# Kernel optimization log

Hardware: AMD Instinct MI355X
Metric: run time of the kernel (lower is better)

Reference implementation:

```python
import jax, jax.numpy as jnp
import numpy as np

D_MODEL = 1024
NHEAD = 16
HEAD_DIM = D_MODEL // NHEAD  # 64
THETA = 10000.0


def apply_rope(t):
    # t: [B, H, S, D]. Interleaved-pair RoPE (lucidrains rotary-embedding-torch
    # rotate_queries_or_keys), positions = arange(S), theta = 10000.
    B, H, S, D = t.shape
    inv_freq = 1.0 / (THETA ** (jnp.arange(0, D, 2, dtype=jnp.float32) / D))  # [D/2]
    ang = jnp.arange(S, dtype=jnp.float32)[:, None] * inv_freq               # [S, D/2]
    cos = jnp.cos(ang).astype(t.dtype)
    sin = jnp.sin(ang).astype(t.dtype)
    tp = t.reshape(B, H, S, D // 2, 2)
    x1, x2 = tp[..., 0], tp[..., 1]
    rot = jnp.stack([x1 * cos - x2 * sin, x1 * sin + x2 * cos], axis=-1)
    return rot.reshape(B, H, S, D)


def setup_inputs() -> dict:
    key = jax.random.key(0)
    k0, k1, k2, k3, k4 = jax.random.split(key, 5)
    B, Sx, Sc = 2, 2048, 2048
    sc = 0.02  # weight init scale
    return {
        "x": jax.random.normal(k0, (B, Sx, D_MODEL), jnp.float32),
        "context": jax.random.normal(k1, (B, Sc, D_MODEL), jnp.float32),
        "Wq": jax.random.normal(k2, (D_MODEL, D_MODEL), jnp.float32) * sc,
        "Wv": jax.random.normal(k3, (D_MODEL, D_MODEL), jnp.float32) * sc,
        "Wo": jax.random.normal(k4, (D_MODEL, D_MODEL), jnp.float32) * sc,
        "bo": jnp.zeros((D_MODEL,), jnp.float32),
        "x_pos": jnp.arange(B * Sx, dtype=jnp.int64).reshape(B, Sx) % Sx,
        "context_pos": jnp.arange(B * Sc, dtype=jnp.int64).reshape(B, Sc) % Sc,
    }


def reference(x, context, Wq, Wv, Wo, bo, x_pos, context_pos):
    # x_pos/context_pos are unused when both streams use the internal
    # RotaryEmbedding (is_imu1=is_imu2=True), matching the original forward.
    B, Sx, _ = x.shape
    Sc = context.shape[1]
    q = (x @ Wq.T).reshape(B, Sx, NHEAD, HEAD_DIM).transpose(0, 2, 1, 3)
    # NOTE: original code uses projq (not projk) for keys — replicated here.
    k = (context @ Wq.T).reshape(B, Sc, NHEAD, HEAD_DIM).transpose(0, 2, 1, 3)
    v = (context @ Wv.T).reshape(B, Sc, NHEAD, HEAD_DIM).transpose(0, 2, 1, 3)
    q = apply_rope(q)
    k = apply_rope(k)
    scale = 1.0 / jnp.sqrt(jnp.asarray(HEAD_DIM, q.dtype))
    attn = jax.nn.softmax(jnp.einsum("bhqd,bhkd->bhqk", q, k) * scale, axis=-1)
    out = jnp.einsum("bhqk,bhkd->bhqd", attn, v)            # [B,H,Sx,hd]
    out = out.transpose(0, 2, 1, 3).reshape(B, Sx, D_MODEL)  # [B,Sx,d_model]
    return out @ Wo.T + bo
```

## Files before the change

### kernel.cpp

```cpp
#include <hip/hip_runtime.h>
#include <cmath>


typedef __bf16 bf16x8 __attribute__((ext_vector_type(8)));
typedef __bf16 bf16x4 __attribute__((ext_vector_type(4)));
typedef float f32x4 __attribute__((ext_vector_type(4)));

#define MFMA(A, B, C) __builtin_amdgcn_mfma_f32_16x16x32_bf16(A, B, C, 0, 0, 0)
#define GLL16(g, l)                                                        \
  __builtin_amdgcn_global_load_lds(                                        \
      (const __attribute__((address_space(1))) unsigned int*)(g),          \
      (__attribute__((address_space(3))) unsigned int*)(l), 16, 0, 0)

__global__ __launch_bounds__(256) void cvt_all_kernel(
    const float* __restrict__ x, const float* __restrict__ ctx,
    const float* __restrict__ Wq, const float* __restrict__ Wv,
    const float* __restrict__ Wo, __bf16* __restrict__ xb, __bf16* __restrict__ cb,
    __bf16* __restrict__ Wqb, __bf16* __restrict__ Wvb, __bf16* __restrict__ Wob) {
  int i = blockIdx.x * 256 + threadIdx.x;
  const float* src;
  __bf16* dst;
  int off;
  if (i < 1048576) { src = x; dst = xb; off = 0; }
  else if (i < 2097152) { src = ctx; dst = cb; off = 1048576; }
  else if (i < 2359296) { src = Wq; dst = Wqb; off = 2097152; }
  else if (i < 2621440) { src = Wv; dst = Wvb; off = 2359296; }
  else { src = Wo; dst = Wob; off = 2621440; }
  int j = i - off;
  float4 f = ((const float4*)src)[j];
  bf16x4 o;
  o[0] = (__bf16)f.x; o[1] = (__bf16)f.y; o[2] = (__bf16)f.z; o[3] = (__bf16)f.w;
  ((bf16x4*)dst)[j] = o;
}

__global__ __launch_bounds__(256) void gemm_proj(const __bf16* __restrict__ A0,
                                                 const __bf16* __restrict__ W0,
                                                 void* __restrict__ outQ,
                                                 void* __restrict__ outK,
                                                 void* __restrict__ outV) {
  const int tid = threadIdx.x;
  const int wave = tid >> 6, lane = tid & 63, quad = lane >> 4, l15 = lane & 15;
  const int mw = wave >> 1, nw = wave & 1;
  const int n0 = blockIdx.y * 128;

  int m0 = blockIdx.x * 128;
  const __bf16* A = A0;
  const __bf16* W = W0;
  bool vmode = false;
  if (blockIdx.x >= 64) {
    m0 = (blockIdx.x - 64) * 128;
    A = A0 + (size_t)4096 * 1024;
    W = W0 + (size_t)1024 * 1024;
    vmode = true;
  }

  __shared__ __attribute__((aligned(16))) __bf16 As[2][4096];
  __shared__ __attribute__((aligned(16))) __bf16 Ws[2][4096];

  int goff[2];
#pragma unroll
  for (int jj = 0; jj < 2; jj++) {
    const int s = jj * 256 + tid;
    const int row = s >> 2;
    const int kcg = (s & 3) ^ ((row >> 1) & 3);
    goff[jj] = row * 1024 + kcg * 8;
  }
  const __bf16* Ag = A + (size_t)m0 * 1024;
  const __bf16* Wg = W + (size_t)n0 * 1024;
  const int ldsoff0 = wave * 512;
  const int ldsoff1 = 2048 + wave * 512;

  const int sw = (l15 >> 1) & 3;
  int afoff[4], wfoff[4];
#pragma unroll
  for (int t = 0; t < 4; t++) {
    afoff[t] = (mw * 64 + t * 16 + l15) * 32 + (quad ^ sw) * 8;
    wfoff[t] = (nw * 64 + t * 16 + l15) * 32 + (quad ^ sw) * 8;
  }

  f32x4 acc[4][4] = {};

  auto stage = [&](int buf, int k0) {
    GLL16(Ag + goff[0] + k0, &As[buf][ldsoff0]);
    GLL16(Ag + goff[1] + k0, &As[buf][ldsoff1]);
    GLL16(Wg + goff[0] + k0, &Ws[buf][ldsoff0]);
    GLL16(Wg + goff[1] + k0, &Ws[buf][ldsoff1]);
  };
  auto compute = [&](int buf) {
    bf16x8 af[4], wf[4];
#pragma unroll
    for (int t = 0; t < 4; t++) af[t] = *(const bf16x8*)&As[buf][afoff[t]];
#pragma unroll
    for (int t = 0; t < 4; t++) wf[t] = *(const bf16x8*)&Ws[buf][wfoff[t]];
#pragma unroll
    for (int mt = 0; mt < 4; mt++)
#pragma unroll
      for (int nt = 0; nt < 4; nt++) acc[mt][nt] = MFMA(af[mt], wf[nt], acc[mt][nt]);
  };

  stage(0, 0);
  for (int k0 = 0; k0 < 1024; k0 += 64) {
    __syncthreads();
    if (k0 + 32 < 1024) stage(1, k0 + 32);
    compute(0);
    __syncthreads();
    if (k0 + 64 < 1024) stage(0, k0 + 64);
    compute(1);
  }

  if (!vmode) {
    const int isK = (m0 >= 4096);
    __bf16* O = (__bf16*)(isK ? outK : outQ);
    const float qsc = isK ? 1.0f : 0.18033688f;
    const int mb = m0 & 4095;
#pragma unroll
    for (int nt = 0; nt < 4; nt++) {
      const int n = n0 + nw * 64 + nt * 16 + l15;
      const int h = n >> 6, d = n & 63, p = d >> 1;
      const float invf = __builtin_amdgcn_exp2f(-(float)p * 0.41524101f);
#pragma unroll
      for (int mt = 0; mt < 4; mt++) {
#pragma unroll
        for (int r = 0; r < 4; r++) {
          const int row = mb + mw * 64 + mt * 16 + quad * 4 + r;
          const int s = row & 2047, b = row >> 11;
          float v = acc[mt][nt][r];
          float pv = __shfl_xor(v, 1, 64);
          float sn, cs;
          __sincosf((float)s * invf, &sn, &cs);
          float res = (lane & 1) ? (pv * sn + v * cs) : (v * cs - pv * sn);
          O[((size_t)(b * 16 + h) * 2048 + s) * 64 + d] = (__bf16)(res * qsc);
        }
      }
    }
  } else {
    __bf16* O = (__bf16*)outV;
#pragma unroll
    for (int nt = 0; nt < 4; nt++) {
      const int n = n0 + nw * 64 + nt * 16 + l15;
      const int h = n >> 6, d = n & 63;
#pragma unroll
      for (int mt = 0; mt < 4; mt++) {
        const int rowb = m0 + mw * 64 + mt * 16 + quad * 4;
        const int s = rowb & 2047, b = rowb >> 11;
        bf16x4 o;
#pragma unroll
        for (int r = 0; r < 4; r++) o[r] = (__bf16)acc[mt][nt][r];
        *(bf16x4*)(O + ((size_t)(b * 16 + h) * 64 + d) * 2048 + s) = o;
      }
    }
  }
}

__global__ __launch_bounds__(256) void gemm_out(const __bf16* __restrict__ A,
                                                const __bf16* __restrict__ W,
                                                float* __restrict__ O,
                                                const float* __restrict__ bias) {
  const int tid = threadIdx.x;
  const int wave = tid >> 6, lane = tid & 63, quad = lane >> 4, l15 = lane & 15;
  const int mw = wave >> 1, nw = wave & 1;
  const int m0 = blockIdx.x * 128, n0 = blockIdx.y * 64;

  __shared__ __attribute__((aligned(16))) __bf16 As[2][4096];
  __shared__ __attribute__((aligned(16))) __bf16 Ws[2][2048];

  int goff[2];
#pragma unroll
  for (int jj = 0; jj < 2; jj++) {
    const int s = jj * 256 + tid;
    const int row = s >> 2;
    const int kcg = (s & 3) ^ ((row >> 1) & 3);
    goff[jj] = row * 1024 + kcg * 8;
  }
  const __bf16* Ag = A + (size_t)m0 * 1024;
  const __bf16* Wg = W + (size_t)n0 * 1024;
  const int ldsoff0 = wave * 512;
  const int ldsoff1 = 2048 + wave * 512;

  const int sw = (l15 >> 1) & 3;
  int afoff[4], wfoff[2];
#pragma unroll
  for (int t = 0; t < 4; t++)
    afoff[t] = (mw * 64 + t * 16 + l15) * 32 + (quad ^ sw) * 8;
#pragma unroll
  for (int t = 0; t < 2; t++)
    wfoff[t] = (nw * 32 + t * 16 + l15) * 32 + (quad ^ sw) * 8;

  f32x4 acc[4][2] = {};

  auto stage = [&](int buf, int k0) {
    GLL16(Ag + goff[0] + k0, &As[buf][ldsoff0]);
    GLL16(Ag + goff[1] + k0, &As[buf][ldsoff1]);
    GLL16(Wg + goff[0] + k0, &Ws[buf][ldsoff0]);
  };
  auto compute = [&](int buf) {
    bf16x8 af[4], wf[2];
#pragma unroll
    for (int t = 0; t < 4; t++) af[t] = *(const bf16x8*)&As[buf][afoff[t]];
#pragma unroll
    for (int t = 0; t < 2; t++) wf[t] = *(const bf16x8*)&Ws[buf][wfoff[t]];
#pragma unroll
    for (int mt = 0; mt < 4; mt++)
#pragma unroll
      for (int nt = 0; nt < 2; nt++) acc[mt][nt] = MFMA(af[mt], wf[nt], acc[mt][nt]);
  };

  stage(0, 0);
  for (int k0 = 0; k0 < 1024; k0 += 64) {
    __syncthreads();
    if (k0 + 32 < 1024) stage(1, k0 + 32);
    compute(0);
    __syncthreads();
    if (k0 + 64 < 1024) stage(0, k0 + 64);
    compute(1);
  }

#pragma unroll
  for (int nt = 0; nt < 2; nt++) {
    const int n = n0 + nw * 32 + nt * 16 + l15;
    const float bv = bias[n];
#pragma unroll
    for (int mt = 0; mt < 4; mt++) {
#pragma unroll
      for (int r = 0; r < 4; r++) {
        const int row = m0 + mw * 64 + mt * 16 + quad * 4 + r;
        O[(size_t)row * 1024 + n] = acc[mt][nt][r] + bv;
      }
    }
  }
}

__global__ __launch_bounds__(256) void attn_kernel(const __bf16* __restrict__ Q,
                                                   const __bf16* __restrict__ K,
                                                   const __bf16* __restrict__ Vt,
                                                   __bf16* __restrict__ Aout) {
  const int tid = threadIdx.x;
  const int wave = tid >> 6, lane = tid & 63, quad = lane >> 4, l15 = lane & 15;
  const int id = blockIdx.x;
  const int j = id >> 3;
  const int bh = ((id & 7) << 2) | (j & 3);
  const int q0 = (j >> 2) << 7;

  const __bf16* Qb = Q + (size_t)bh * (2048 * 64);
  const __bf16* Kb = K + (size_t)bh * (2048 * 64);
  const __bf16* Vb = Vt + (size_t)bh * (64 * 2048);

  __shared__ __attribute__((aligned(16))) __bf16 Kbuf[2][4096];
  __shared__ __attribute__((aligned(16))) __bf16 Vbuf[2][4096];
  __shared__ __attribute__((aligned(16))) __bf16 Plds[4][2][8][16][8];

  bf16x8 qf[2][2];
#pragma unroll
  for (int c = 0; c < 2; c++) {
    const __bf16* qp = Qb + (size_t)(q0 + wave * 32 + c * 16 + l15) * 64 + quad * 8;
    qf[c][0] = *(const bf16x8*)qp;
    qf[c][1] = *(const bf16x8*)(qp + 32);
  }

  const int s0 = (wave * 2 + 0) * 64 + lane;
  const int s1 = (wave * 2 + 1) * 64 + lane;
  const int r0 = s0 >> 3, c0 = (s0 & 7) ^ (r0 & 7);
  const int r1 = s1 >> 3, c1 = (s1 & 7) ^ (r1 & 7);
  const __bf16* kg0 = Kb + r0 * 64 + c0 * 8;
  const __bf16* kg1 = Kb + r1 * 64 + c1 * 8;
  const __bf16* vg0 = Vb + r0 * 2048 + c0 * 8;
  const __bf16* vg1 = Vb + r1 * 2048 + c1 * 8;
  const int kldsA = (wave * 2 + 0) * 512;
  const int kldsB = (wave * 2 + 1) * 512;

  const int offF0 = l15 * 64 + ((quad ^ (l15 & 7)) * 8);
  const int offF1 = l15 * 64 + (((4 + quad) ^ (l15 & 7)) * 8);

  float rsum[2] = {0.f, 0.f};
  f32x4 oT[4][2] = {};

  auto stage = [&](int buf, int kt) {
    GLL16(kg0 + kt * 64, &Kbuf[buf][kldsA]);
    GLL16(kg1 + kt * 64, &Kbuf[buf][kldsB]);
    GLL16(vg0 + kt, &Vbuf[buf][kldsA]);
    GLL16(vg1 + kt, &Vbuf[buf][kldsB]);
  };
  auto compute = [&](int buf) {
    f32x4 sT[2][4];
#pragma unroll
    for (int nt = 0; nt < 4; nt++) {
      bf16x8 kf0 = *(const bf16x8*)&Kbuf[buf][nt * 1024 + offF0];
      bf16x8 kf1 = *(const bf16x8*)&Kbuf[buf][nt * 1024 + offF1];
#pragma unroll
      for (int c = 0; c < 2; c++) {
        f32x4 z = {};
        z = MFMA(kf0, qf[c][0], z);
        sT[c][nt] = MFMA(kf1, qf[c][1], z);
      }
    }
#pragma unroll
    for (int c = 0; c < 2; c++) {
#pragma unroll
      for (int nt = 0; nt < 4; nt++) {
        bf16x4 pb;
#pragma unroll
        for (int r = 0; r < 4; r++) {
          float pe = __builtin_amdgcn_exp2f(sT[c][nt][r]);
          rsum[c] += pe;
          pb[r] = (__bf16)pe;
        }
        const int chunk = nt * 2 + (quad >> 1);
        *(bf16x4*)&Plds[wave][c][chunk][l15 ^ ((chunk & 3) << 1)][(quad & 1) * 4] = pb;
      }
    }
    bf16x8 pf[2][2];
#pragma unroll
    for (int c = 0; c < 2; c++) {
      pf[c][0] = *(const bf16x8*)&Plds[wave][c][quad][l15 ^ (quad << 1)][0];
      pf[c][1] = *(const bf16x8*)&Plds[wave][c][4 + quad][l15 ^ (quad << 1)][0];
    }
#pragma unroll
    for (int nt = 0; nt < 4; nt++) {
      bf16x8 vf0 = *(const bf16x8*)&Vbuf[buf][nt * 1024 + offF0];
      bf16x8 vf1 = *(const bf16x8*)&Vbuf[buf][nt * 1024 + offF1];
#pragma unroll
      for (int c = 0; c < 2; c++) {
        oT[nt][c] = MFMA(vf0, pf[c][0], oT[nt][c]);
        oT[nt][c] = MFMA(vf1, pf[c][1], oT[nt][c]);
      }
    }
  };

  stage(0, 0);
  for (int kt = 0; kt < 2048; kt += 128) {
    __syncthreads();
    if (kt + 64 < 2048) stage(1, kt + 64);
    compute(0);
    __syncthreads();
    if (kt + 128 < 2048) stage(0, kt + 128);
    compute(1);
  }

  const int b = bh >> 4, h = bh & 15;
#pragma unroll
  for (int c = 0; c < 2; c++) {
    float l = rsum[c];
    l += __shfl_xor(l, 16, 64);
    l += __shfl_xor(l, 32, 64);
    const float inv = 1.f / l;
    const int q = q0 + wave * 32 + c * 16 + l15;
#pragma unroll
    for (int nt = 0; nt < 4; nt++) {
      bf16x4 o;
#pragma unroll
      for (int r = 0; r < 4; r++) o[r] = (__bf16)(oT[nt][c][r] * inv);
      *(bf16x4*)&Aout[((size_t)(b * 2048 + q)) * 1024 + h * 64 + nt * 16 + quad * 4] = o;
    }
  }
}

extern "C" void kernel_launch(void* const* d_in, const int* in_sizes, int n_in,
                              void* d_out, int out_size, void* d_ws, size_t ws_size,
                              hipStream_t stream) {
  const float* x   = (const float*)d_in[0];
  const float* ctx = (const float*)d_in[1];
  const float* Wq  = (const float*)d_in[2];
  const float* Wv  = (const float*)d_in[3];
  const float* Wo  = (const float*)d_in[4];
  const float* bo  = (const float*)d_in[5];

  char* ws = (char*)d_ws;
  const size_t MB = 1024 * 1024;
  __bf16* xb   = (__bf16*)(ws + 0 * MB);
  __bf16* cb   = (__bf16*)(ws + 8 * MB);
  __bf16* Wqb  = (__bf16*)(ws + 16 * MB);
  __bf16* Wvb  = (__bf16*)(ws + 18 * MB);
  __bf16* Wob  = (__bf16*)(ws + 20 * MB);
  __bf16* qh   = (__bf16*)(ws + 22 * MB);
  __bf16* kh   = (__bf16*)(ws + 30 * MB);
  __bf16* vt   = (__bf16*)(ws + 38 * MB);
  __bf16* attn = xb;

  cvt_all_kernel<<<11264, 256, 0, stream>>>(x, ctx, Wq, Wv, Wo, xb, cb, Wqb, Wvb, Wob);

  gemm_proj<<<dim3(96, 8), 256, 0, stream>>>(xb, Wqb, (void*)qh, (void*)kh, (void*)vt);

  attn_kernel<<<512, 256, 0, stream>>>(qh, kh, vt, attn);

  gemm_out<<<dim3(32, 16), 256, 0, stream>>>(attn, Wob, (float*)d_out, bo);
}
```

Before: 216.2 us.

## Retune conversion, RoPE trig, output GEMM tiling, and attention pipelining

```diff
diff --git a/kernel.cpp b/kernel.cpp
--- a/kernel.cpp
+++ b/kernel.cpp
@@ -17,20 +17,23 @@
     const float* __restrict__ Wq, const float* __restrict__ Wv,
     const float* __restrict__ Wo, __bf16* __restrict__ xb, __bf16* __restrict__ cb,
     __bf16* __restrict__ Wqb, __bf16* __restrict__ Wvb, __bf16* __restrict__ Wob) {
-  int i = blockIdx.x * 256 + threadIdx.x;
+  int base = blockIdx.x * 512 + threadIdx.x;
   const float* src;
   __bf16* dst;
   int off;
-  if (i < 1048576) { src = x; dst = xb; off = 0; }
-  else if (i < 2097152) { src = ctx; dst = cb; off = 1048576; }
-  else if (i < 2359296) { src = Wq; dst = Wqb; off = 2097152; }
-  else if (i < 2621440) { src = Wv; dst = Wvb; off = 2359296; }
+  if (base < 1048576) { src = x; dst = xb; off = 0; }
+  else if (base < 2097152) { src = ctx; dst = cb; off = 1048576; }
+  else if (base < 2359296) { src = Wq; dst = Wqb; off = 2097152; }
+  else if (base < 2621440) { src = Wv; dst = Wvb; off = 2359296; }
   else { src = Wo; dst = Wob; off = 2621440; }
-  int j = i - off;
-  float4 f = ((const float4*)src)[j];
-  bf16x4 o;
-  o[0] = (__bf16)f.x; o[1] = (__bf16)f.y; o[2] = (__bf16)f.z; o[3] = (__bf16)f.w;
-  ((bf16x4*)dst)[j] = o;
+#pragma unroll
+  for (int jj = 0; jj < 2; jj++) {
+    int j = base - off + jj * 256;
+    float4 f = ((const float4*)src)[j];
+    bf16x4 o;
+    o[0] = (__bf16)f.x; o[1] = (__bf16)f.y; o[2] = (__bf16)f.z; o[3] = (__bf16)f.w;
+    ((bf16x4*)dst)[j] = o;
+  }
 }
 
 __global__ __launch_bounds__(256) void gemm_proj(const __bf16* __restrict__ A0,
@@ -117,7 +120,8 @@
     for (int nt = 0; nt < 4; nt++) {
       const int n = n0 + nw * 64 + nt * 16 + l15;
       const int h = n >> 6, d = n & 63, p = d >> 1;
-      const float invf = __builtin_amdgcn_exp2f(-(float)p * 0.41524101f);
+      const float invf_rev =
+          __builtin_amdgcn_exp2f(-((float)p * 0.41524101f + 2.6514961f));
 #pragma unroll
       for (int mt = 0; mt < 4; mt++) {
 #pragma unroll
@@ -126,8 +130,9 @@
           const int s = row & 2047, b = row >> 11;
           float v = acc[mt][nt][r];
           float pv = __shfl_xor(v, 1, 64);
-          float sn, cs;
-          __sincosf((float)s * invf, &sn, &cs);
+          float fr = __builtin_amdgcn_fractf((float)s * invf_rev);
+          float sn = __builtin_amdgcn_sinf(fr);
+          float cs = __builtin_amdgcn_cosf(fr);
           float res = (lane & 1) ? (pv * sn + v * cs) : (v * cs - pv * sn);
           O[((size_t)(b * 16 + h) * 2048 + s) * 64 + d] = (__bf16)(res * qsc);
         }
@@ -159,48 +164,39 @@
   const int tid = threadIdx.x;
   const int wave = tid >> 6, lane = tid & 63, quad = lane >> 4, l15 = lane & 15;
   const int mw = wave >> 1, nw = wave & 1;
-  const int m0 = blockIdx.x * 128, n0 = blockIdx.y * 64;
-
-  __shared__ __attribute__((aligned(16))) __bf16 As[2][4096];
+  const int m0 = blockIdx.x * 64, n0 = blockIdx.y * 64;
+
+  __shared__ __attribute__((aligned(16))) __bf16 As[2][2048];
   __shared__ __attribute__((aligned(16))) __bf16 Ws[2][2048];
 
-  int goff[2];
-#pragma unroll
-  for (int jj = 0; jj < 2; jj++) {
-    const int s = jj * 256 + tid;
-    const int row = s >> 2;
-    const int kcg = (s & 3) ^ ((row >> 1) & 3);
-    goff[jj] = row * 1024 + kcg * 8;
-  }
+  const int srow = tid >> 2;
+  const int goff = srow * 1024 + (((tid & 3) ^ ((srow >> 1) & 3)) * 8);
   const __bf16* Ag = A + (size_t)m0 * 1024;
   const __bf16* Wg = W + (size_t)n0 * 1024;
-  const int ldsoff0 = wave * 512;
-  const int ldsoff1 = 2048 + wave * 512;
+  const int ldsoff = wave * 512;
 
   const int sw = (l15 >> 1) & 3;
-  int afoff[4], wfoff[2];
-#pragma unroll
-  for (int t = 0; t < 4; t++)
-    afoff[t] = (mw * 64 + t * 16 + l15) * 32 + (quad ^ sw) * 8;
-#pragma unroll
-  for (int t = 0; t < 2; t++)
+  int afoff[2], wfoff[2];
+#pragma unroll
+  for (int t = 0; t < 2; t++) {
+    afoff[t] = (mw * 32 + t * 16 + l15) * 32 + (quad ^ sw) * 8;
     wfoff[t] = (nw * 32 + t * 16 + l15) * 32 + (quad ^ sw) * 8;
-
-  f32x4 acc[4][2] = {};
+  }
+
+  f32x4 acc[2][2] = {};
 
   auto stage = [&](int buf, int k0) {
-    GLL16(Ag + goff[0] + k0, &As[buf][ldsoff0]);
-    GLL16(Ag + goff[1] + k0, &As[buf][ldsoff1]);
-    GLL16(Wg + goff[0] + k0, &Ws[buf][ldsoff0]);
+    GLL16(Ag + goff + k0, &As[buf][ldsoff]);
+    GLL16(Wg + goff + k0, &Ws[buf][ldsoff]);
   };
   auto compute = [&](int buf) {
-    bf16x8 af[4], wf[2];
-#pragma unroll
-    for (int t = 0; t < 4; t++) af[t] = *(const bf16x8*)&As[buf][afoff[t]];
+    bf16x8 af[2], wf[2];
+#pragma unroll
+    for (int t = 0; t < 2; t++) af[t] = *(const bf16x8*)&As[buf][afoff[t]];
 #pragma unroll
     for (int t = 0; t < 2; t++) wf[t] = *(const bf16x8*)&Ws[buf][wfoff[t]];
 #pragma unroll
-    for (int mt = 0; mt < 4; mt++)
+    for (int mt = 0; mt < 2; mt++)
 #pragma unroll
       for (int nt = 0; nt < 2; nt++) acc[mt][nt] = MFMA(af[mt], wf[nt], acc[mt][nt]);
   };
@@ -220,10 +216,10 @@
     const int n = n0 + nw * 32 + nt * 16 + l15;
     const float bv = bias[n];
 #pragma unroll
-    for (int mt = 0; mt < 4; mt++) {
+    for (int mt = 0; mt < 2; mt++) {
 #pragma unroll
       for (int r = 0; r < 4; r++) {
-        const int row = m0 + mw * 64 + mt * 16 + quad * 4 + r;
+        const int row = m0 + mw * 32 + mt * 16 + quad * 4 + r;
         O[(size_t)row * 1024 + n] = acc[mt][nt][r] + bv;
       }
     }
@@ -245,8 +241,8 @@
   const __bf16* Kb = K + (size_t)bh * (2048 * 64);
   const __bf16* Vb = Vt + (size_t)bh * (64 * 2048);
 
-  __shared__ __attribute__((aligned(16))) __bf16 Kbuf[2][4096];
-  __shared__ __attribute__((aligned(16))) __bf16 Vbuf[2][4096];
+  __shared__ __attribute__((aligned(16))) __bf16 Kbuf[4][4096];
+  __shared__ __attribute__((aligned(16))) __bf16 Vbuf[4][4096];
   __shared__ __attribute__((aligned(16))) __bf16 Plds[4][2][8][16][8];
 
   bf16x8 qf[2][2];
@@ -271,7 +267,7 @@
   const int offF0 = l15 * 64 + ((quad ^ (l15 & 7)) * 8);
   const int offF1 = l15 * 64 + (((4 + quad) ^ (l15 & 7)) * 8);
 
-  float rsum[2] = {0.f, 0.f};
+  f32x4 rs4[2] = {};
   f32x4 oT[4][2] = {};
 
   auto stage = [&](int buf, int kt) {
@@ -298,12 +294,13 @@
 #pragma unroll
       for (int nt = 0; nt < 4; nt++) {
         bf16x4 pb;
+        f32x4 pe;
 #pragma unroll
         for (int r = 0; r < 4; r++) {
-          float pe = __builtin_amdgcn_exp2f(sT[c][nt][r]);
-          rsum[c] += pe;
-          pb[r] = (__bf16)pe;
+          pe[r] = __builtin_amdgcn_exp2f(sT[c][nt][r]);
+          pb[r] = (__bf16)pe[r];
         }
+        rs4[c] += pe;
         const int chunk = nt * 2 + (quad >> 1);
         *(bf16x4*)&Plds[wave][c][chunk][l15 ^ ((chunk & 3) << 1)][(quad & 1) * 4] = pb;
       }
@@ -327,19 +324,22 @@
   };
 
   stage(0, 0);
+  stage(1, 64);
   for (int kt = 0; kt < 2048; kt += 128) {
-    __syncthreads();
-    if (kt + 64 < 2048) stage(1, kt + 64);
-    compute(0);
-    __syncthreads();
-    if (kt + 128 < 2048) stage(0, kt + 128);
-    compute(1);
+    const int p = (kt >> 7) & 1;
+    __syncthreads();
+    if (kt + 128 < 2048) {
+      stage(2 * (p ^ 1), kt + 128);
+      stage(2 * (p ^ 1) + 1, kt + 192);
+    }
+    compute(2 * p);
+    compute(2 * p + 1);
   }
 
   const int b = bh >> 4, h = bh & 15;
 #pragma unroll
   for (int c = 0; c < 2; c++) {
-    float l = rsum[c];
+    float l = (rs4[c][0] + rs4[c][1]) + (rs4[c][2] + rs4[c][3]);
     l += __shfl_xor(l, 16, 64);
     l += __shfl_xor(l, 32, 64);
     const float inv = 1.f / l;
@@ -376,11 +376,11 @@
   __bf16* vt   = (__bf16*)(ws + 38 * MB);
   __bf16* attn = xb;
 
-  cvt_all_kernel<<<11264, 256, 0, stream>>>(x, ctx, Wq, Wv, Wo, xb, cb, Wqb, Wvb, Wob);
+  cvt_all_kernel<<<5632, 256, 0, stream>>>(x, ctx, Wq, Wv, Wo, xb, cb, Wqb, Wvb, Wob);
 
   gemm_proj<<<dim3(96, 8), 256, 0, stream>>>(xb, Wqb, (void*)qh, (void*)kh, (void*)vt);
 
   attn_kernel<<<512, 256, 0, stream>>>(qh, kh, vt, attn);
 
-  gemm_out<<<dim3(32, 16), 256, 0, stream>>>(attn, Wob, (float*)d_out, bo);
-}
+  gemm_out<<<dim3(64, 16), 256, 0, stream>>>(attn, Wob, (float*)d_out, bo);
+}
```

After: 209.6 us. 3.1% less time.
